# Performance work log

Measured on AMD Instinct MI355X. Metric: run time of the kernel, lower is better.

## Reference

```python
import jax, jax.numpy as jnp
import numpy as np

N_ENT, N_REL, RANK, B = 40000, 1200, 200, 500
INIT = 1e-3


def _lorentz_rotate(lhs, rot):
    # lhs: [B, d, 5], rot: [B, d, 4]; quaternion rotation of spatial part
    rot = jax.nn.gelu(rot, approximate=False)  # torch F.gelu default = exact erf
    t, r, i, j, k = (lhs[..., m:m + 1] for m in range(5))
    rr, ri, rj, rk = (rot[..., m:m + 1] for m in range(4))
    A = r * rr - i * ri - j * rj - k * rk
    Bq = r * ri + rr * i + j * rk - rj * k
    C = r * rj + rr * j + k * ri - rk * i
    D = r * rk + rr * k + i * rj - ri * j
    return jnp.concatenate([t, A, Bq, C, D], axis=-1)


def _lorentz_boost2(lhs, boost):
    # lhs: [B, d, 5], boost: [B, d, 4]
    b = jax.nn.sigmoid(boost) / 4.0
    t, s = lhs[..., 0:1], lhs[..., 1:]               # [B,d,1], [B,d,4]
    b2 = jnp.sum(b * b, axis=-1, keepdims=True)      # [B,d,1]
    eye = jnp.eye(4, dtype=lhs.dtype)
    bb = jnp.sqrt(eye + b[..., :, None] * b[..., None, :])  # [B,d,4,4]
    xt = t * b2 + jnp.sum(b * s, axis=-1, keepdims=True)
    xs = t * b + jnp.einsum('bdij,bdj->bdi', bb, s)
    return jnp.concatenate([xt, xs], axis=-1)


def setup_inputs() -> dict:
    key = jax.random.key(0)
    k1, k2, k3, k4 = jax.random.split(key, 4)
    ent = jax.random.normal(k1, (N_ENT, RANK, 5), jnp.float32) * INIT
    ent = ent / jnp.linalg.norm(ent, axis=-1, keepdims=True)  # param_init normalization
    rot = jax.random.normal(k2, (N_REL, RANK, 4), jnp.float32) * INIT
    boo = jax.random.normal(k3, (N_REL, RANK, 4), jnp.float32) * INIT
    queries = jax.random.randint(k4, (B, 3), 0, 1000, jnp.int32)
    return {'queries': queries, 'ent_embedding': ent, 'rel_rotate': rot, 'rel_boosts': boo}


def reference(queries, ent_embedding, rel_rotate, rel_boosts):
    lhs = ent_embedding[queries[:, 0]]     # [B, d, 5]
    rot = rel_rotate[queries[:, 1]]        # [B, d, 4]
    boost = rel_boosts[queries[:, 1]]      # [B, d, 4]
    lhs = _lorentz_rotate(lhs, rot)
    lhs = _lorentz_boost2(lhs, boost)
    # cinner: negate time component of x, contract over (d,5), mean over d
    x = lhs.at[..., 0].multiply(-1.0)
    d = ent_embedding.shape[1]
    cin = jnp.einsum('bdi,ndi->bn', x, ent_embedding) / d  # [B, n_ent]
    scores = 2.0 + 2.0 * cin  # -( -2 - 2*cinner )
    reg_rel = jnp.sqrt(jnp.sum(rot ** 2, axis=-1)) + jnp.sqrt(jnp.sum(boost ** 2, axis=-1))
    return scores, reg_rel
```

## Files before the change

### kernel.cpp

```cpp
#include <hip/hip_runtime.h>
#include <hip/hip_bf16.h>
#include <math.h>

#define N_ENT   40000
#define RANK    200
#define NB      500
#define K_REAL  1000
#define K_PAD   1024
#define M_PAD   512

typedef __attribute__((ext_vector_type(8))) short       short8;
typedef __attribute__((ext_vector_type(4))) float       f32x4;
typedef __attribute__((ext_vector_type(8))) unsigned short ushort8v;

__device__ __forceinline__ unsigned short f2bf(float f) {
    union { float f; unsigned int u; } v; v.f = f;
    unsigned int u = v.u;
    return (unsigned short)((u + 0x7FFFu + ((u >> 16) & 1u)) >> 16);
}

__device__ __forceinline__ unsigned int pack_hi(float x, float y) {
    return (__float_as_uint(x) >> 16) | (__float_as_uint(y) & 0xFFFF0000u);
}

__device__ __forceinline__ void gld_lds16(const void* g, void* l) {
    __builtin_amdgcn_global_load_lds(
        (const __attribute__((address_space(1))) unsigned int*)g,
        (__attribute__((address_space(3))) unsigned int*)l,
        16, 0, 0);
}

__global__ __launch_bounds__(256) void lkg_prep(
    const int* __restrict__ queries,
    const float* __restrict__ ent,
    const float* __restrict__ rot,
    const float* __restrict__ boo,
    unsigned short* __restrict__ xws,
    float* __restrict__ out)
{
    const int b   = blockIdx.x;
    const int tid = threadIdx.x;
    unsigned short* xrow = xws + (size_t)b * K_PAD;

    if (b >= NB) {
        ((uint2*)xrow)[tid] = make_uint2(0u, 0u);
        return;
    }
    if (tid >= RANK) {
        int c = tid - RANK;
        if (c < K_PAD - K_REAL) xrow[K_REAL + c] = 0;
        return;
    }

    const int d  = tid;
    const int q0 = queries[b * 3 + 0];
    const int q1 = queries[b * 3 + 1];

    const float* L  = ent + (size_t)q0 * (RANK * 5) + d * 5;
    const float* R  = rot + (size_t)q1 * (RANK * 4) + d * 4;
    const float* Bo = boo + (size_t)q1 * (RANK * 4) + d * 4;

    const float t = L[0], r = L[1], i = L[2], j = L[3], k = L[4];
    const float r0 = R[0],  r1 = R[1],  r2 = R[2],  r3 = R[3];
    const float o0 = Bo[0], o1 = Bo[1], o2 = Bo[2], o3 = Bo[3];

    out[(size_t)NB * N_ENT + (size_t)b * RANK + d] =
        sqrtf(r0*r0 + r1*r1 + r2*r2 + r3*r3) +
        sqrtf(o0*o0 + o1*o1 + o2*o2 + o3*o3);

    const float is2 = 0.70710678118654752440f;
    const float rr = 0.5f * r0 * (1.0f + erff(r0 * is2));
    const float ri = 0.5f * r1 * (1.0f + erff(r1 * is2));
    const float rj = 0.5f * r2 * (1.0f + erff(r2 * is2));
    const float rk = 0.5f * r3 * (1.0f + erff(r3 * is2));

    const float s0 = r*rr - i*ri - j*rj - k*rk;
    const float s1 = r*ri + rr*i + j*rk - rj*k;
    const float s2 = r*rj + rr*j + k*ri - rk*i;
    const float s3 = r*rk + rr*k + i*rj - ri*j;

    const float b0 = 0.25f / (1.0f + expf(-o0));
    const float b1 = 0.25f / (1.0f + expf(-o1));
    const float b2 = 0.25f / (1.0f + expf(-o2));
    const float b3 = 0.25f / (1.0f + expf(-o3));

    const float bsq = b0*b0 + b1*b1 + b2*b2 + b3*b3;
    const float xt  = t * bsq + b0*s0 + b1*s1 + b2*s2 + b3*s3;

    const float m00 = sqrtf(1.0f + b0*b0), m11 = sqrtf(1.0f + b1*b1);
    const float m22 = sqrtf(1.0f + b2*b2), m33 = sqrtf(1.0f + b3*b3);
    const float m01 = sqrtf(b0*b1), m02 = sqrtf(b0*b2), m03 = sqrtf(b0*b3);
    const float m12 = sqrtf(b1*b2), m13 = sqrtf(b1*b3), m23 = sqrtf(b2*b3);

    const float xs0 = t*b0 + m00*s0 + m01*s1 + m02*s2 + m03*s3;
    const float xs1 = t*b1 + m01*s0 + m11*s1 + m12*s2 + m13*s3;
    const float xs2 = t*b2 + m02*s0 + m12*s1 + m22*s2 + m23*s3;
    const float xs3 = t*b3 + m03*s0 + m13*s1 + m23*s2 + m33*s3;

    unsigned short* w = xrow + d * 5;
    w[0] = f2bf(-xt);
    w[1] = f2bf(xs0);
    w[2] = f2bf(xs1);
    w[3] = f2bf(xs2);
    w[4] = f2bf(xs3);
}

__global__ __launch_bounds__(256) void lkg_gemm4(
    const unsigned short* __restrict__ xbf,
    const float* __restrict__ ent,
    float* __restrict__ out)
{
    __shared__ __align__(16) unsigned char smx[24576];
    unsigned short* As  = (unsigned short*)smx;
    float*          Bsf = (float*)(smx + 8192);

    const int bm  = blockIdx.x;
    const int n0  = blockIdx.y * 128;
    const int tid = threadIdx.x;
    const int wave = tid >> 6, lane = tid & 63;
    const int wy = wave >> 1, wx = wave & 1;
    const int l15 = lane & 15, quad = lane >> 4;

    f32x4 acc[4][4] = {};

    for (int kt = 0; kt < 32; ++kt) {
        #pragma unroll
        for (int ii = 0; ii < 2; ++ii) {
            const int c = tid + ii * 256;
            const int row = c >> 2, cc = c & 3;
            const int ksw = cc ^ ((row >> 1) & 3);
            gld_lds16(xbf + (size_t)(bm * 128 + row) * K_PAD + kt * 32 + ksw * 8,
                      (void*)(As + c * 8));
        }
        if (kt < 31) {
            #pragma unroll
            for (int ii = 0; ii < 4; ++ii) {
                const int c = tid + ii * 256;
                const int row = c >> 3, cc = c & 7;
                const int ksw = cc ^ (row & 7);
                const int gr  = (n0 + row < N_ENT) ? (n0 + row) : (N_ENT - 1);
                gld_lds16(ent + (size_t)gr * K_REAL + kt * 32 + ksw * 4,
                          (void*)(Bsf + c * 4));
            }
        } else if (tid < 128) {
            const int row = tid;
            const int gr  = (n0 + row < N_ENT) ? (n0 + row) : (N_ENT - 1);
            const float4 v0 = *(const float4*)(ent + (size_t)gr * K_REAL + 992);
            const float4 v1 = *(const float4*)(ent + (size_t)gr * K_REAL + 996);
            *(float4*)(Bsf + row * 32 + (0 ^ (row & 7)) * 4) = v0;
            *(float4*)(Bsf + row * 32 + (1 ^ (row & 7)) * 4) = v1;
        }
        __syncthreads();

        short8 a[4], bfr[4];
        #pragma unroll
        for (int mi = 0; mi < 4; ++mi) {
            const int row = wy * 64 + mi * 16 + l15;
            a[mi] = *(const short8*)(As + row * 32 + (quad ^ ((row >> 1) & 3)) * 8);
        }
        #pragma unroll
        for (int ni = 0; ni < 4; ++ni) {
            const int row = wx * 64 + ni * 16 + l15;
            const int sw  = row & 7;
            const float4 c0 = *(const float4*)(Bsf + row * 32 + ((2 * quad)     ^ sw) * 4);
            const float4 c1 = *(const float4*)(Bsf + row * 32 + ((2 * quad + 1) ^ sw) * 4);
            union { unsigned int u[4]; short8 s; } pk;
            pk.u[0] = pack_hi(c0.x, c0.y);
            pk.u[1] = pack_hi(c0.z, c0.w);
            pk.u[2] = pack_hi(c1.x, c1.y);
            pk.u[3] = pack_hi(c1.z, c1.w);
            bfr[ni] = pk.s;
        }

        #pragma unroll
        for (int mi = 0; mi < 4; ++mi)
            #pragma unroll
            for (int ni = 0; ni < 4; ++ni)
                acc[mi][ni] = __builtin_amdgcn_mfma_f32_16x16x32_bf16(
                    a[mi], bfr[ni], acc[mi][ni], 0, 0, 0);

        __syncthreads();
    }

    const int EPLD = 132;
    float* ep = (float*)smx;
    #pragma unroll
    for (int mi = 0; mi < 4; ++mi) {
        if (mi) __syncthreads();
        #pragma unroll
        for (int ni = 0; ni < 4; ++ni)
            #pragma unroll
            for (int r = 0; r < 4; ++r)
                ep[(wy * 16 + quad * 4 + r) * EPLD + wx * 64 + ni * 16 + l15] =
                    acc[mi][ni][r];
        __syncthreads();
        #pragma unroll
        for (int p = 0; p < 4; ++p) {
            const int lrow = (tid >> 5) + p * 8;
            const int col  = (tid & 31) * 4;
            const int wyy = lrow >> 4, within = lrow & 15;
            const int grow = bm * 128 + wyy * 64 + mi * 16 + within;
            if (grow < NB && n0 + col < N_ENT) {
                const float4 v = *(const float4*)(ep + lrow * EPLD + col);
                float4 o;
                o.x = 2.0f + 0.01f * v.x; o.y = 2.0f + 0.01f * v.y;
                o.z = 2.0f + 0.01f * v.z; o.w = 2.0f + 0.01f * v.w;
                *(float4*)(out + (size_t)grow * N_ENT + n0 + col) = o;
            }
        }
    }
}

extern "C" void kernel_launch(void* const* d_in, const int* in_sizes, int n_in,
                              void* d_out, int out_size, void* d_ws, size_t ws_size,
                              hipStream_t stream) {
    const int*   queries = (const int*)d_in[0];
    const float* ent     = (const float*)d_in[1];
    const float* rot     = (const float*)d_in[2];
    const float* boo     = (const float*)d_in[3];
    float*       out     = (float*)d_out;
    unsigned short* xbf  = (unsigned short*)d_ws;

    lkg_prep<<<M_PAD, 256, 0, stream>>>(queries, ent, rot, boo, xbf, out);
    lkg_gemm4<<<dim3(4, (N_ENT + 127) / 128), 256, 0, stream>>>(xbf, ent, out);
}
```

Before: 337.6 us.

## Tile GEMM over full M per block with double-buffered LDS pipeline

Each block now processes all 512 query rows against a 64-entity slice, so the fp32 entity matrix is streamed once instead of once per M tile. LDS is double-buffered so the next K tile's async loads overlap the current MFMA work. The K tail is handled by clamping load offsets against zero-padded A columns. The cost is re-reading the small bf16 query matrix per block and using 80KB LDS, which limits occupancy.

```diff
diff --git a/kernel.cpp b/kernel.cpp
--- a/kernel.cpp
+++ b/kernel.cpp
@@ -11,7 +11,6 @@
 
 typedef __attribute__((ext_vector_type(8))) short       short8;
 typedef __attribute__((ext_vector_type(4))) float       f32x4;
-typedef __attribute__((ext_vector_type(8))) unsigned short ushort8v;
 
 __device__ __forceinline__ unsigned short f2bf(float f) {
     union { float f; unsigned int u; } v; v.f = f;
@@ -105,84 +104,83 @@
     w[4] = f2bf(xs3);
 }
 
-__global__ __launch_bounds__(256) void lkg_gemm4(
+__global__ __launch_bounds__(512, 4) void lkg_gemm5(
     const unsigned short* __restrict__ xbf,
     const float* __restrict__ ent,
     float* __restrict__ out)
 {
-    __shared__ __align__(16) unsigned char smx[24576];
-    unsigned short* As  = (unsigned short*)smx;
-    float*          Bsf = (float*)(smx + 8192);
-
-    const int bm  = blockIdx.x;
-    const int n0  = blockIdx.y * 128;
-    const int tid = threadIdx.x;
+    __shared__ __align__(16) unsigned char smx[2 * 40960];
+
+    const int n0   = blockIdx.x * 64;
+    const int tid  = threadIdx.x;
     const int wave = tid >> 6, lane = tid & 63;
-    const int wy = wave >> 1, wx = wave & 1;
-    const int l15 = lane & 15, quad = lane >> 4;
+    const int l15  = lane & 15, quad = lane >> 4;
 
     f32x4 acc[4][4] = {};
 
-    for (int kt = 0; kt < 32; ++kt) {
-        #pragma unroll
-        for (int ii = 0; ii < 2; ++ii) {
-            const int c = tid + ii * 256;
+    auto stage = [&](int kt, unsigned char* smbuf) {
+        unsigned short* As = (unsigned short*)smbuf;
+        float*          Bs = (float*)(smbuf + 32768);
+        #pragma unroll
+        for (int ii = 0; ii < 4; ++ii) {
+            const int c   = tid + ii * 512;
             const int row = c >> 2, cc = c & 3;
             const int ksw = cc ^ ((row >> 1) & 3);
-            gld_lds16(xbf + (size_t)(bm * 128 + row) * K_PAD + kt * 32 + ksw * 8,
+            gld_lds16(xbf + (size_t)row * K_PAD + kt * 32 + ksw * 8,
                       (void*)(As + c * 8));
         }
-        if (kt < 31) {
-            #pragma unroll
-            for (int ii = 0; ii < 4; ++ii) {
-                const int c = tid + ii * 256;
-                const int row = c >> 3, cc = c & 7;
-                const int ksw = cc ^ (row & 7);
-                const int gr  = (n0 + row < N_ENT) ? (n0 + row) : (N_ENT - 1);
-                gld_lds16(ent + (size_t)gr * K_REAL + kt * 32 + ksw * 4,
-                          (void*)(Bsf + c * 4));
-            }
-        } else if (tid < 128) {
-            const int row = tid;
-            const int gr  = (n0 + row < N_ENT) ? (n0 + row) : (N_ENT - 1);
-            const float4 v0 = *(const float4*)(ent + (size_t)gr * K_REAL + 992);
-            const float4 v1 = *(const float4*)(ent + (size_t)gr * K_REAL + 996);
-            *(float4*)(Bsf + row * 32 + (0 ^ (row & 7)) * 4) = v0;
-            *(float4*)(Bsf + row * 32 + (1 ^ (row & 7)) * 4) = v1;
-        }
-        __syncthreads();
-
-        short8 a[4], bfr[4];
+        {
+            const int c   = tid;
+            const int row = c >> 3, cc = c & 7;
+            const int ksw = cc ^ (row & 7);
+            int ko = kt * 32 + ksw * 4;
+            if (ko > K_REAL - 4) ko = K_REAL - 4;
+            gld_lds16(ent + (size_t)(n0 + row) * K_REAL + ko,
+                      (void*)(Bs + c * 4));
+        }
+    };
+
+    auto compute = [&](const unsigned char* smbuf) {
+        const unsigned short* As = (const unsigned short*)smbuf;
+        const float*          Bs = (const float*)(smbuf + 32768);
+        short8 a[4], b[4];
         #pragma unroll
         for (int mi = 0; mi < 4; ++mi) {
-            const int row = wy * 64 + mi * 16 + l15;
+            const int row = wave * 64 + mi * 16 + l15;
             a[mi] = *(const short8*)(As + row * 32 + (quad ^ ((row >> 1) & 3)) * 8);
         }
         #pragma unroll
         for (int ni = 0; ni < 4; ++ni) {
-            const int row = wx * 64 + ni * 16 + l15;
+            const int row = ni * 16 + l15;
             const int sw  = row & 7;
-            const float4 c0 = *(const float4*)(Bsf + row * 32 + ((2 * quad)     ^ sw) * 4);
-            const float4 c1 = *(const float4*)(Bsf + row * 32 + ((2 * quad + 1) ^ sw) * 4);
+            const float4 c0 = *(const float4*)(Bs + row * 32 + ((2 * quad)     ^ sw) * 4);
+            const float4 c1 = *(const float4*)(Bs + row * 32 + ((2 * quad + 1) ^ sw) * 4);
             union { unsigned int u[4]; short8 s; } pk;
             pk.u[0] = pack_hi(c0.x, c0.y);
             pk.u[1] = pack_hi(c0.z, c0.w);
             pk.u[2] = pack_hi(c1.x, c1.y);
             pk.u[3] = pack_hi(c1.z, c1.w);
-            bfr[ni] = pk.s;
-        }
-
+            b[ni] = pk.s;
+        }
         #pragma unroll
         for (int mi = 0; mi < 4; ++mi)
             #pragma unroll
             for (int ni = 0; ni < 4; ++ni)
                 acc[mi][ni] = __builtin_amdgcn_mfma_f32_16x16x32_bf16(
-                    a[mi], bfr[ni], acc[mi][ni], 0, 0, 0);
-
+                    a[mi], b[ni], acc[mi][ni], 0, 0, 0);
+    };
+
+    stage(0, smx);
+    __syncthreads();
+
+    for (int kt = 0; kt < 31; ++kt) {
+        stage(kt + 1, smx + ((kt + 1) & 1) * 40960);
+        compute(smx + (kt & 1) * 40960);
         __syncthreads();
     }
-
-    const int EPLD = 132;
+    compute(smx + 40960);
+
+    const int EPS = 68;
     float* ep = (float*)smx;
     #pragma unroll
     for (int mi = 0; mi < 4; ++mi) {
@@ -191,21 +189,21 @@
         for (int ni = 0; ni < 4; ++ni)
             #pragma unroll
             for (int r = 0; r < 4; ++r)
-                ep[(wy * 16 + quad * 4 + r) * EPLD + wx * 64 + ni * 16 + l15] =
+                ep[(wave * 16 + quad * 4 + r) * EPS + ni * 16 + l15] =
                     acc[mi][ni][r];
         __syncthreads();
         #pragma unroll
         for (int p = 0; p < 4; ++p) {
-            const int lrow = (tid >> 5) + p * 8;
-            const int col  = (tid & 31) * 4;
-            const int wyy = lrow >> 4, within = lrow & 15;
-            const int grow = bm * 128 + wyy * 64 + mi * 16 + within;
-            if (grow < NB && n0 + col < N_ENT) {
-                const float4 v = *(const float4*)(ep + lrow * EPLD + col);
+            const int idx  = p * 512 + tid;
+            const int lrow = idx >> 4;
+            const int c4   = idx & 15;
+            const int grow = (lrow >> 4) * 64 + mi * 16 + (lrow & 15);
+            if (grow < NB) {
+                const float4 v = *(const float4*)(ep + lrow * EPS + c4 * 4);
                 float4 o;
                 o.x = 2.0f + 0.01f * v.x; o.y = 2.0f + 0.01f * v.y;
                 o.z = 2.0f + 0.01f * v.z; o.w = 2.0f + 0.01f * v.w;
-                *(float4*)(out + (size_t)grow * N_ENT + n0 + col) = o;
+                *(float4*)(out + (size_t)grow * N_ENT + n0 + c4 * 4) = o;
             }
         }
     }
@@ -222,5 +220,5 @@
     unsigned short* xbf  = (unsigned short*)d_ws;
 
     lkg_prep<<<M_PAD, 256, 0, stream>>>(queries, ent, rot, boo, xbf, out);
-    lkg_gemm4<<<dim3(4, (N_ENT + 127) / 128), 256, 0, stream>>>(xbf, ent, out);
-}
+    lkg_gemm5<<<dim3(625), 512, 0, stream>>>(xbf, ent, out);
+}
```

Result: slower. 367.2 us (+8.8%).
